# Kernel tuning notes

Measured on AMD Instinct MI355X. Metric: run time of the kernel, lower is better.

Reference implementation:

```python
import jax, jax.numpy as jnp
import numpy as np


def setup_inputs() -> dict:
    key = jax.random.key(0)
    kq, kk, kv = jax.random.split(key, 3)
    N, L, S, H, D = 4, 2048, 2048, 8, 64
    queries = jax.random.normal(kq, (N, L, H, D), dtype=jnp.float32)
    keys = jax.random.normal(kk, (N, S, H, D), dtype=jnp.float32)
    values = jax.random.normal(kv, (N, S, H, D), dtype=jnp.float32)
    return {"queries": queries, "keys": keys, "values": values}


def reference(queries, keys, values):
    # QK^T: [N, L, S, H]
    qk = jnp.einsum('nlhd,nshd->nlsh', queries, keys)
    softmax_temp = 1.0 / np.sqrt(queries.shape[3]).astype(np.float32)
    attn = jax.nn.softmax(softmax_temp * qk, axis=2)  # softmax over S
    # dropout with drop_rate=0.0 is identity
    out = jnp.einsum('nlsh,nshd->nlhd', attn, values)
    return out
```

## Files before the change

kernel.cpp:

```cpp
#include <hip/hip_runtime.h>
#include <hip/hip_bf16.h>
#include <stdint.h>


typedef __bf16 bf16x8 __attribute__((ext_vector_type(8)));
typedef __bf16 bf16x4 __attribute__((ext_vector_type(4)));
typedef float  f32x16 __attribute__((ext_vector_type(16)));

#define N_ 4
#define L_ 2048
#define S_ 2048
#define H_ 8
#define D_ 64
#define NH 32
#define QBLK 128
#define KVBLK 64
#define NKV (S_ / KVBLK)
#define HEAD_ELEMS (S_ * D_)
#define SCALE_LOG2E 0.18033688011112042f

typedef const __attribute__((address_space(1))) uint8_t* gptr_t;
typedef __attribute__((address_space(3))) uint8_t* lptr_t;
#define GLOAD16(g, l) __builtin_amdgcn_global_load_lds((gptr_t)(g), (lptr_t)(l), 16, 0, 0)

static __device__ __forceinline__ uint32_t pkbf(float lo, float hi) {
    uint16_t l = __builtin_bit_cast(uint16_t, (__bf16)lo);
    uint16_t h = __builtin_bit_cast(uint16_t, (__bf16)hi);
    return (uint32_t)l | ((uint32_t)h << 16);
}

__global__ __launch_bounds__(256) void prep_k(const float* __restrict__ K,
                                              __bf16* __restrict__ Kb) {
    const int chunk = blockIdx.x * 256 + threadIdx.x;
    const int n     = chunk >> 18;
    const int rem   = chunk & 262143;
    const int s     = rem >> 7;
    const int r2    = rem & 127;
    const int h     = r2 >> 4;
    const int dslot = r2 & 15;
    float4 v = *(const float4*)(K + (size_t)chunk * 4);
    bf16x4 o = { (__bf16)v.x, (__bf16)v.y, (__bf16)v.z, (__bf16)v.w };
    *(bf16x4*)(Kb + ((size_t)(n * 8 + h) * 2048 + s) * 64 + dslot * 4) = o;
}

__global__ __launch_bounds__(256) void prep_v(const float* __restrict__ V,
                                              __bf16* __restrict__ Vt) {
    __shared__ __align__(16) __bf16 T[64 * 64];
    const int tid = threadIdx.x;
    const int bid = blockIdx.x;
    const int nh  = bid >> 5;
    const int n   = nh >> 3, h = nh & 7;
    const int s0  = (bid & 31) * 64;
#pragma unroll
    for (int it = 0; it < 16; ++it) {
        const int idx = it * 256 + tid;
        const int sl  = idx >> 6;
        const int d   = idx & 63;
        float v = V[(size_t)(n * 2048 + s0 + sl) * 512 + h * 64 + d];
        T[d * 64 + (((sl >> 3) ^ (d & 7)) * 8) + (sl & 7)] = (__bf16)v;
    }
    __syncthreads();
#pragma unroll
    for (int it = 0; it < 2; ++it) {
        const int idx = it * 256 + tid;
        const int d   = idx >> 3;
        const int sc  = idx & 7;
        bf16x8 v = *(const bf16x8*)&T[d * 64 + ((sc ^ (d & 7)) * 8)];
        *(bf16x8*)(Vt + (size_t)nh * HEAD_ELEMS + (size_t)d * 2048 + s0 + sc * 8) = v;
    }
}

__global__ __launch_bounds__(256, 2) void fattn(const float* __restrict__ Q,
                                                const __bf16* __restrict__ Kb,
                                                const __bf16* __restrict__ Vt,
                                                float* __restrict__ Out) {
    __shared__ __align__(16) __bf16 Kl[2][KVBLK * 64];
    __shared__ __align__(16) __bf16 Vl[2][64 * KVBLK];

    const int tid  = threadIdx.x;
    const int wave = tid >> 6;
    const int lane = tid & 63;
    const int hh   = lane >> 5;
    const int c    = lane & 31;

    int bid = blockIdx.x;
    bid = (bid & 7) * 64 + (bid >> 3);
    const int nh = bid >> 4;
    const int qt = bid & 15;
    const int n  = nh >> 3, hd = nh & 7;
    const int q0 = qt * QBLK;

    const float*  Qp = Q   + (size_t)n * 1048576 + hd * 64;
    float*        Op = Out + (size_t)n * 1048576 + hd * 64;
    const __bf16* Kh = Kb + (size_t)nh * HEAD_ELEMS;
    const __bf16* Vh = Vt + (size_t)nh * HEAD_ELEMS;

    int koff[2], voff[2], ldst[2];
#pragma unroll
    for (int c2 = 0; c2 < 2; ++c2) {
        const int slot = wave * 128 + c2 * 64 + lane;
        const int row  = slot >> 3, sc = slot & 7;
        koff[c2] = row * 64   + ((sc ^ (row & 7)) * 8);
        voff[c2] = row * 2048 + ((sc ^ (row & 7)) * 8);
        ldst[c2] = (wave * 128 + c2 * 64) * 8;
    }

    bf16x8 qf[4];
    {
        const float* qp = Qp + (size_t)(q0 + wave * 32 + c) * 512;
#pragma unroll
        for (int ks = 0; ks < 4; ++ks) {
            float4 a = *(const float4*)(qp + ks * 16 + hh * 8);
            float4 b = *(const float4*)(qp + ks * 16 + hh * 8 + 4);
            bf16x8 v;
            v[0] = (__bf16)(a.x * SCALE_LOG2E); v[1] = (__bf16)(a.y * SCALE_LOG2E);
            v[2] = (__bf16)(a.z * SCALE_LOG2E); v[3] = (__bf16)(a.w * SCALE_LOG2E);
            v[4] = (__bf16)(b.x * SCALE_LOG2E); v[5] = (__bf16)(b.y * SCALE_LOG2E);
            v[6] = (__bf16)(b.z * SCALE_LOG2E); v[7] = (__bf16)(b.w * SCALE_LOG2E);
            qf[ks] = v;
        }
    }

    auto stage = [&](int b, int kv) {
        const __bf16* kbase = Kh + (size_t)kv * 4096;
        const __bf16* vbase = Vh + kv * 64;
#pragma unroll
        for (int c2 = 0; c2 < 2; ++c2) {
            GLOAD16(kbase + koff[c2], &Kl[b][ldst[c2]]);
            GLOAD16(vbase + voff[c2], &Vl[b][ldst[c2]]);
        }
    };

    float m_r = -1e30f, lsum = 0.f;
    f32x16 oacc[2];
#pragma unroll
    for (int dt = 0; dt < 2; ++dt)
#pragma unroll
        for (int r = 0; r < 16; ++r) oacc[dt][r] = 0.f;

    stage(0, 0);
    __syncthreads();
    int buf = 0;

    for (int kv = 0; kv < NKV; ++kv) {
        if (kv + 1 < NKV) stage(buf ^ 1, kv + 1);

        f32x16 sacc[2];
#pragma unroll
        for (int st = 0; st < 2; ++st)
#pragma unroll
            for (int r = 0; r < 16; ++r) sacc[st][r] = 0.f;

        __builtin_amdgcn_s_setprio(1);
#pragma unroll
        for (int ks = 0; ks < 4; ++ks) {
#pragma unroll
            for (int st = 0; st < 2; ++st) {
                bf16x8 kf = *(const bf16x8*)&Kl[buf][(st * 32 + c) * 64 + (((ks * 2 + hh) ^ (c & 7)) * 8)];
                sacc[st] = __builtin_amdgcn_mfma_f32_32x32x16_bf16(kf, qf[ks], sacc[st], 0, 0, 0);
            }
        }
        __builtin_amdgcn_s_setprio(0);

        float tm = sacc[0][0];
#pragma unroll
        for (int r = 1; r < 16; ++r) tm = fmaxf(tm, sacc[0][r]);
#pragma unroll
        for (int r = 0; r < 16; ++r) tm = fmaxf(tm, sacc[1][r]);
        tm = fmaxf(tm, __shfl_xor(tm, 32, 64));
        if (!__all(tm <= m_r + 8.0f)) {
            const float mnew = fmaxf(m_r, tm);
            const float al   = __builtin_amdgcn_exp2f(m_r - mnew);
            m_r = mnew;
            lsum *= al;
#pragma unroll
            for (int dt = 0; dt < 2; ++dt)
#pragma unroll
                for (int r = 0; r < 16; ++r) oacc[dt][r] *= al;
        }
        float ps = 0.f;
#pragma unroll
        for (int st = 0; st < 2; ++st)
#pragma unroll
            for (int r = 0; r < 16; ++r) {
                const float p = __builtin_amdgcn_exp2f(sacc[st][r] - m_r);
                sacc[st][r] = p;
                ps += p;
            }
        lsum += ps;

        bf16x8 pf[4];
#pragma unroll
        for (int st = 0; st < 2; ++st) {
            uint32_t W[8];
#pragma unroll
            for (int i = 0; i < 8; ++i) W[i] = pkbf(sacc[st][2 * i], sacc[st][2 * i + 1]);
#pragma unroll
            for (int kk = 0; kk < 2; ++kk) {
                uint32_t a0 = W[4 * kk + 0], b0 = W[4 * kk + 2];
                uint32_t a1 = W[4 * kk + 1], b1 = W[4 * kk + 3];
                asm volatile("v_permlane32_swap_b32 %0, %1" : "+v"(a0), "+v"(b0));
                asm volatile("v_permlane32_swap_b32 %0, %1" : "+v"(a1), "+v"(b1));
                union { uint32_t u[4]; bf16x8 v; } pu;
                pu.u[0] = a0; pu.u[1] = a1; pu.u[2] = b0; pu.u[3] = b1;
                pf[st * 2 + kk] = pu.v;
            }
        }

        __builtin_amdgcn_s_setprio(1);
#pragma unroll
        for (int kt = 0; kt < 4; ++kt) {
#pragma unroll
            for (int dt = 0; dt < 2; ++dt) {
                bf16x8 vf = *(const bf16x8*)&Vl[buf][(dt * 32 + c) * 64 + (((kt * 2 + hh) ^ (c & 7)) * 8)];
                oacc[dt] = __builtin_amdgcn_mfma_f32_32x32x16_bf16(vf, pf[kt], oacc[dt], 0, 0, 0);
            }
        }
        __builtin_amdgcn_s_setprio(0);

        __syncthreads();
        buf ^= 1;
    }

    lsum += __shfl_xor(lsum, 32, 64);
    const float inv = 1.0f / lsum;
    float* op = Op + (size_t)(q0 + wave * 32 + c) * 512;
#pragma unroll
    for (int dt = 0; dt < 2; ++dt) {
#pragma unroll
        for (int rr = 0; rr < 4; ++rr) {
            float4 o = { oacc[dt][4 * rr + 0] * inv, oacc[dt][4 * rr + 1] * inv,
                         oacc[dt][4 * rr + 2] * inv, oacc[dt][4 * rr + 3] * inv };
            *(float4*)(op + dt * 32 + rr * 8 + hh * 4) = o;
        }
    }
}

extern "C" void kernel_launch(void* const* d_in, const int* in_sizes, int n_in,
                              void* d_out, int out_size, void* d_ws, size_t ws_size,
                              hipStream_t stream) {
    const float* Q = (const float*)d_in[0];
    const float* K = (const float*)d_in[1];
    const float* V = (const float*)d_in[2];
    float* Out = (float*)d_out;
    __bf16* Kb = (__bf16*)d_ws;
    __bf16* Vt = Kb + (size_t)NH * HEAD_ELEMS;

    prep_k<<<dim3(4096), dim3(256), 0, stream>>>(K, Kb);
    prep_v<<<dim3(1024), dim3(256), 0, stream>>>(V, Vt);
    fattn <<<dim3(512),  dim3(256), 0, stream>>>(Q, Kb, Vt, Out);
}
```

Before: 75.53 us.

## Pre-swizzle K/V into MFMA fragment order and load directly to registers

The prep kernels now write K and V into one interleaved per-head plane laid out in the exact per-lane MFMA fragment order, 8 KB of K then 8 KB of V per 64-row tile. The attention kernel drops LDS staging and the per-iteration __syncthreads. Each wave loads its K/V fragments straight from global memory (L2) into registers, with software double-buffering of K across an unrolled pair of iterations. The row max and row sum reductions become trees. Every wave now redundantly fetches the full K/V tile from cache instead of sharing it through LDS, and register pressure rises.

```diff
diff --git a/kernel.cpp b/kernel.cpp
--- a/kernel.cpp
+++ b/kernel.cpp
@@ -4,7 +4,6 @@
 
 
 typedef __bf16 bf16x8 __attribute__((ext_vector_type(8)));
-typedef __bf16 bf16x4 __attribute__((ext_vector_type(4)));
 typedef float  f32x16 __attribute__((ext_vector_type(16)));
 
 #define N_ 4
@@ -15,13 +14,10 @@
 #define NH 32
 #define QBLK 128
 #define KVBLK 64
-#define NKV (S_ / KVBLK)
-#define HEAD_ELEMS (S_ * D_)
+#define NKV 32
+#define TILE_BF16 8192
+#define PLANE_BF16 (NKV * TILE_BF16)
 #define SCALE_LOG2E 0.18033688011112042f
-
-typedef const __attribute__((address_space(1))) uint8_t* gptr_t;
-typedef __attribute__((address_space(3))) uint8_t* lptr_t;
-#define GLOAD16(g, l) __builtin_amdgcn_global_load_lds((gptr_t)(g), (lptr_t)(l), 16, 0, 0)
 
 static __device__ __forceinline__ uint32_t pkbf(float lo, float hi) {
     uint16_t l = __builtin_bit_cast(uint16_t, (__bf16)lo);
@@ -30,27 +26,34 @@
 }
 
 __global__ __launch_bounds__(256) void prep_k(const float* __restrict__ K,
-                                              __bf16* __restrict__ Kb) {
-    const int chunk = blockIdx.x * 256 + threadIdx.x;
-    const int n     = chunk >> 18;
-    const int rem   = chunk & 262143;
-    const int s     = rem >> 7;
-    const int r2    = rem & 127;
-    const int h     = r2 >> 4;
-    const int dslot = r2 & 15;
-    float4 v = *(const float4*)(K + (size_t)chunk * 4);
-    bf16x4 o = { (__bf16)v.x, (__bf16)v.y, (__bf16)v.z, (__bf16)v.w };
-    *(bf16x4*)(Kb + ((size_t)(n * 8 + h) * 2048 + s) * 64 + dslot * 4) = o;
+                                              __bf16* __restrict__ F) {
+    const int ch   = blockIdx.x * 256 + threadIdx.x;
+    const int nh   = ch >> 14;
+    const int kv   = (ch >> 9) & 31;
+    const int r    = ch & 511;
+    const int sl   = r >> 3;
+    const int slot = r & 7;
+    const int n = nh >> 3, h = nh & 7;
+    const float* p = K + ((size_t)(n * 2048 + kv * 64 + sl) * 8 + h) * 64 + slot * 8;
+    float4 a = *(const float4*)p;
+    float4 b = *(const float4*)(p + 4);
+    bf16x8 v;
+    v[0] = (__bf16)a.x; v[1] = (__bf16)a.y; v[2] = (__bf16)a.z; v[3] = (__bf16)a.w;
+    v[4] = (__bf16)b.x; v[5] = (__bf16)b.y; v[6] = (__bf16)b.z; v[7] = (__bf16)b.w;
+    const int st = sl >> 5, c = sl & 31, ks = slot >> 1, hh = slot & 1;
+    *(bf16x8*)(F + (size_t)nh * PLANE_BF16 + kv * TILE_BF16
+                 + (st * 4 + ks) * 512 + (hh * 32 + c) * 8) = v;
 }
 
 __global__ __launch_bounds__(256) void prep_v(const float* __restrict__ V,
-                                              __bf16* __restrict__ Vt) {
+                                              __bf16* __restrict__ F) {
     __shared__ __align__(16) __bf16 T[64 * 64];
     const int tid = threadIdx.x;
     const int bid = blockIdx.x;
     const int nh  = bid >> 5;
+    const int kv  = bid & 31;
     const int n   = nh >> 3, h = nh & 7;
-    const int s0  = (bid & 31) * 64;
+    const int s0  = kv * 64;
 #pragma unroll
     for (int it = 0; it < 16; ++it) {
         const int idx = it * 256 + tid;
@@ -66,17 +69,15 @@
         const int d   = idx >> 3;
         const int sc  = idx & 7;
         bf16x8 v = *(const bf16x8*)&T[d * 64 + ((sc ^ (d & 7)) * 8)];
-        *(bf16x8*)(Vt + (size_t)nh * HEAD_ELEMS + (size_t)d * 2048 + s0 + sc * 8) = v;
+        const int dt = d >> 5, c = d & 31, kt = sc >> 1, hh = sc & 1;
+        *(bf16x8*)(F + (size_t)nh * PLANE_BF16 + kv * TILE_BF16
+                     + (8 + dt * 4 + kt) * 512 + (hh * 32 + c) * 8) = v;
     }
 }
 
 __global__ __launch_bounds__(256, 2) void fattn(const float* __restrict__ Q,
-                                                const __bf16* __restrict__ Kb,
-                                                const __bf16* __restrict__ Vt,
+                                                const __bf16* __restrict__ F,
                                                 float* __restrict__ Out) {
-    __shared__ __align__(16) __bf16 Kl[2][KVBLK * 64];
-    __shared__ __align__(16) __bf16 Vl[2][64 * KVBLK];
-
     const int tid  = threadIdx.x;
     const int wave = tid >> 6;
     const int lane = tid & 63;
@@ -92,18 +93,7 @@
 
     const float*  Qp = Q   + (size_t)n * 1048576 + hd * 64;
     float*        Op = Out + (size_t)n * 1048576 + hd * 64;
-    const __bf16* Kh = Kb + (size_t)nh * HEAD_ELEMS;
-    const __bf16* Vh = Vt + (size_t)nh * HEAD_ELEMS;
-
-    int koff[2], voff[2], ldst[2];
-#pragma unroll
-    for (int c2 = 0; c2 < 2; ++c2) {
-        const int slot = wave * 128 + c2 * 64 + lane;
-        const int row  = slot >> 3, sc = slot & 7;
-        koff[c2] = row * 64   + ((sc ^ (row & 7)) * 8);
-        voff[c2] = row * 2048 + ((sc ^ (row & 7)) * 8);
-        ldst[c2] = (wave * 128 + c2 * 64) * 8;
-    }
+    const __bf16* Pl = F + (size_t)nh * PLANE_BF16;
 
     bf16x8 qf[4];
     {
@@ -121,16 +111,6 @@
         }
     }
 
-    auto stage = [&](int b, int kv) {
-        const __bf16* kbase = Kh + (size_t)kv * 4096;
-        const __bf16* vbase = Vh + kv * 64;
-#pragma unroll
-        for (int c2 = 0; c2 < 2; ++c2) {
-            GLOAD16(kbase + koff[c2], &Kl[b][ldst[c2]]);
-            GLOAD16(vbase + voff[c2], &Vl[b][ldst[c2]]);
-        }
-    };
-
     float m_r = -1e30f, lsum = 0.f;
     f32x16 oacc[2];
 #pragma unroll
@@ -138,36 +118,41 @@
 #pragma unroll
         for (int r = 0; r < 16; ++r) oacc[dt][r] = 0.f;
 
-    stage(0, 0);
-    __syncthreads();
-    int buf = 0;
-
-    for (int kv = 0; kv < NKV; ++kv) {
-        if (kv + 1 < NKV) stage(buf ^ 1, kv + 1);
-
+    bf16x8 kA[8], kB[8], vv[8];
+
+    auto LK = [&](bf16x8 (&dst)[8], int kv) {
+        const bf16x8* t = (const bf16x8*)(Pl + (size_t)kv * TILE_BF16);
+#pragma unroll
+        for (int f = 0; f < 8; ++f) dst[f] = t[f * 64 + lane];
+    };
+    auto LV = [&](bf16x8 (&dst)[8], int kv) {
+        const bf16x8* t = (const bf16x8*)(Pl + (size_t)kv * TILE_BF16) + 512;
+#pragma unroll
+        for (int f = 0; f < 8; ++f) dst[f] = t[f * 64 + lane];
+    };
+
+    auto ITER = [&](bf16x8 (&kf)[8], bf16x8 (&vf)[8]) {
         f32x16 sacc[2];
 #pragma unroll
         for (int st = 0; st < 2; ++st)
 #pragma unroll
             for (int r = 0; r < 16; ++r) sacc[st][r] = 0.f;
-
         __builtin_amdgcn_s_setprio(1);
 #pragma unroll
-        for (int ks = 0; ks < 4; ++ks) {
-#pragma unroll
-            for (int st = 0; st < 2; ++st) {
-                bf16x8 kf = *(const bf16x8*)&Kl[buf][(st * 32 + c) * 64 + (((ks * 2 + hh) ^ (c & 7)) * 8)];
-                sacc[st] = __builtin_amdgcn_mfma_f32_32x32x16_bf16(kf, qf[ks], sacc[st], 0, 0, 0);
-            }
-        }
+        for (int ks = 0; ks < 4; ++ks)
+#pragma unroll
+            for (int st = 0; st < 2; ++st)
+                sacc[st] = __builtin_amdgcn_mfma_f32_32x32x16_bf16(kf[st * 4 + ks], qf[ks], sacc[st], 0, 0, 0);
         __builtin_amdgcn_s_setprio(0);
 
-        float tm = sacc[0][0];
-#pragma unroll
-        for (int r = 1; r < 16; ++r) tm = fmaxf(tm, sacc[0][r]);
-#pragma unroll
-        for (int r = 0; r < 16; ++r) tm = fmaxf(tm, sacc[1][r]);
-        tm = fmaxf(tm, __shfl_xor(tm, 32, 64));
+        float mx[16];
+#pragma unroll
+        for (int i = 0; i < 16; ++i) mx[i] = fmaxf(sacc[0][i], sacc[1][i]);
+#pragma unroll
+        for (int w = 8; w >= 1; w >>= 1)
+#pragma unroll
+            for (int i = 0; i < w; ++i) mx[i] = fmaxf(mx[i], mx[i + w]);
+        float tm = fmaxf(mx[0], __shfl_xor(mx[0], 32, 64));
         if (!__all(tm <= m_r + 8.0f)) {
             const float mnew = fmaxf(m_r, tm);
             const float al   = __builtin_amdgcn_exp2f(m_r - mnew);
@@ -178,16 +163,19 @@
 #pragma unroll
                 for (int r = 0; r < 16; ++r) oacc[dt][r] *= al;
         }
-        float ps = 0.f;
 #pragma unroll
         for (int st = 0; st < 2; ++st)
 #pragma unroll
-            for (int r = 0; r < 16; ++r) {
-                const float p = __builtin_amdgcn_exp2f(sacc[st][r] - m_r);
-                sacc[st][r] = p;
-                ps += p;
-            }
-        lsum += ps;
+            for (int r = 0; r < 16; ++r)
+                sacc[st][r] = __builtin_amdgcn_exp2f(sacc[st][r] - m_r);
+        float sm[16];
+#pragma unroll
+        for (int i = 0; i < 16; ++i) sm[i] = sacc[0][i] + sacc[1][i];
+#pragma unroll
+        for (int w = 8; w >= 1; w >>= 1)
+#pragma unroll
+            for (int i = 0; i < w; ++i) sm[i] += sm[i + w];
+        lsum += sm[0];
 
         bf16x8 pf[4];
 #pragma unroll
@@ -209,17 +197,21 @@
 
         __builtin_amdgcn_s_setprio(1);
 #pragma unroll
-        for (int kt = 0; kt < 4; ++kt) {
-#pragma unroll
-            for (int dt = 0; dt < 2; ++dt) {
-                bf16x8 vf = *(const bf16x8*)&Vl[buf][(dt * 32 + c) * 64 + (((kt * 2 + hh) ^ (c & 7)) * 8)];
-                oacc[dt] = __builtin_amdgcn_mfma_f32_32x32x16_bf16(vf, pf[kt], oacc[dt], 0, 0, 0);
-            }
-        }
+        for (int kt = 0; kt < 4; ++kt)
+#pragma unroll
+            for (int dt = 0; dt < 2; ++dt)
+                oacc[dt] = __builtin_amdgcn_mfma_f32_32x32x16_bf16(vf[dt * 4 + kt], pf[kt], oacc[dt], 0, 0, 0);
         __builtin_amdgcn_s_setprio(0);
-
-        __syncthreads();
-        buf ^= 1;
+    };
+
+    LK(kA, 0);
+    for (int kv = 0; kv < NKV; kv += 2) {
+        LV(vv, kv);
+        LK(kB, kv + 1);
+        ITER(kA, vv);
+        LV(vv, kv + 1);
+        LK(kA, kv + 2 < NKV ? kv + 2 : NKV - 1);
+        ITER(kB, vv);
     }
 
     lsum += __shfl_xor(lsum, 32, 64);
@@ -243,10 +235,9 @@
     const float* K = (const float*)d_in[1];
     const float* V = (const float*)d_in[2];
     float* Out = (float*)d_out;
-    __bf16* Kb = (__bf16*)d_ws;
-    __bf16* Vt = Kb + (size_t)NH * HEAD_ELEMS;
-
-    prep_k<<<dim3(4096), dim3(256), 0, stream>>>(K, Kb);
-    prep_v<<<dim3(1024), dim3(256), 0, stream>>>(V, Vt);
-    fattn <<<dim3(512),  dim3(256), 0, stream>>>(Q, Kb, Vt, Out);
-}
+    __bf16* F = (__bf16*)d_ws;
+
+    prep_k<<<dim3(2048), dim3(256), 0, stream>>>(K, F);
+    prep_v<<<dim3(1024), dim3(256), 0, stream>>>(V, F);
+    fattn <<<dim3(512),  dim3(256), 0, stream>>>(Q, F, Out);
+}
```

Result: faster. 70.95 us (-6.1%).
